# Kernel optimization log

Measured on AMD Instinct MI355X. Metric: run time of the kernel, lower is better.

The kernel has to match this reference:

```python
import jax, jax.numpy as jnp
import numpy as np

C = 64

def _dwconv3d(x, w, b, tdil):
    # x: (B,C,T,H,W); w: (C,1,3,3,3) depthwise; temporal dilation tdil, padding (tdil,1,1)
    y = jax.lax.conv_general_dilated(
        x, w,
        window_strides=(1, 1, 1),
        padding=((tdil, tdil), (1, 1), (1, 1)),
        rhs_dilation=(tdil, 1, 1),
        dimension_numbers=('NCDHW', 'OIDHW', 'NCDHW'),
        feature_group_count=x.shape[1],
    )
    return y + b[None, :, None, None, None]

def _lag_diff(x, k):
    # first k frames kept, rest = x[t] - x[t-k]  (vectorized, no Python loop over T)
    return jnp.concatenate([x[:, :, :k], x[:, :, k:] - x[:, :, :-k]], axis=2)

def setup_inputs() -> dict:
    key = jax.random.key(0)
    ks = jax.random.split(key, 8)
    B, T, H, W = 4, 32, 56, 56
    s = 0.05
    inp = {
        'input': jax.random.normal(ks[0], (B, C, T, H, W), dtype=jnp.float32),
        'w1': jax.random.normal(ks[1], (C, 1, 3, 3, 3), dtype=jnp.float32) * s,
        'b1': jax.random.normal(ks[2], (C,), dtype=jnp.float32) * s,
        'w2': jax.random.normal(ks[3], (C, 1, 3, 3, 3), dtype=jnp.float32) * s,
        'b2': jax.random.normal(ks[4], (C,), dtype=jnp.float32) * s,
        'w3': jax.random.normal(ks[5], (C, 1, 3, 3, 3), dtype=jnp.float32) * s,
        'b3': jax.random.normal(ks[6], (C,), dtype=jnp.float32) * s,
        'weights': jnp.ones((3,), dtype=jnp.float32) / 3.0,
    }
    return inp

def reference(input, w1, b1, w2, b2, w3, b3, weights):
    d1 = _lag_diff(_dwconv3d(input, w1, b1, 1), 1)
    d2 = _lag_diff(_dwconv3d(input, w2, b2, 2), 2)
    d3 = _lag_diff(_dwconv3d(input, w3, b3, 3), 3)
    half = jnp.float32(0.5)
    gate = ((jax.nn.sigmoid(d1) - half) * weights[0]
            + (jax.nn.sigmoid(d2) - half) * weights[1]
            + (jax.nn.sigmoid(d3) - half) * weights[2])
    return input * gate
```

## Files before the change

kernel.cpp:

```cpp
#include <hip/hip_runtime.h>

namespace {

constexpr int T = 32, H = 56, W = 56;
constexpr int HW = H * W;
constexpr int THW = T * HW;
constexpr int PAIRS = HW / 2;
constexpr int BLK = 256;
constexpr int BLOCKS_PER_BC = (PAIRS + BLK - 1) / BLK;

template <int N> struct ic { static constexpr int value = N; };

__device__ __forceinline__ float sigm(float x) {
    float e = __expf(-x);
    return __builtin_amdgcn_rcpf(1.0f + e);
}

__global__ __launch_bounds__(BLK, 4)
void tts_fused(const float* __restrict__ x,
               const float* __restrict__ w1, const float* __restrict__ b1,
               const float* __restrict__ w2, const float* __restrict__ b2,
               const float* __restrict__ w3, const float* __restrict__ b3,
               const float* __restrict__ wm,
               float* __restrict__ out) {
    const int bid = blockIdx.x;
    const int bc  = bid / BLOCKS_PER_BC;
    const int sub = bid - bc * BLOCKS_PER_BC;
    const int q   = sub * BLK + threadIdx.x;
    if (q >= PAIRS) return;
    const int px0 = q * 2;
    const int h   = px0 / W;
    const int w0  = px0 - h * W;

    const float* __restrict__ xbc = x + (size_t)bc * THW;
    float* __restrict__ obc       = out + (size_t)bc * THW;
    const int c = bc & 63;
    const float* __restrict__ wa = w1 + c * 27;
    const float* __restrict__ wb = w2 + c * 27;
    const float* __restrict__ wc = w3 + c * 27;
    const float bias1 = b1[c], bias2 = b2[c], bias3 = b3[c];
    const float W0 = wm[0], W1 = wm[1], W2 = wm[2];
    const float goff = 0.5f * (W0 + W1 + W2);

    const bool vtop = (h >= 1), vbot = (h <= H - 2);
    const bool vl = (w0 > 0), vr = (w0 < W - 2);
    const int boff = h * W + w0;

    float cc[7][3][4];
    float p1[2], p2a[2], p2b[2], p3a[2], p3b[2], p3c[2];
#pragma unroll
    for (int p = 0; p < 2; ++p) {
        p1[p] = 0.f; p2a[p] = 0.f; p2b[p] = 0.f;
        p3a[p] = 0.f; p3b[p] = 0.f; p3c[p] = 0.f;
    }

    auto zero_plane = [&](auto Sc) {
        constexpr int s = decltype(Sc)::value;
#pragma unroll
        for (int r = 0; r < 3; ++r)
#pragma unroll
            for (int j = 0; j < 4; ++j) cc[s][r][j] = 0.f;
    };

    auto load_plane = [&](auto Sc, int tp) {
        constexpr int s = decltype(Sc)::value;
        const float* pp = xbc + tp * HW + boff;
#pragma unroll
        for (int r = 0; r < 3; ++r) {
            const bool vrow = (r == 0) ? vtop : ((r == 2) ? vbot : true);
            const float* rp = pp + (r - 1) * W;
            if (vrow) {
                const float2 m = *(const float2*)rp;
                cc[s][r][1] = m.x; cc[s][r][2] = m.y;
                cc[s][r][0] = vl ? rp[-1] : 0.f;
                cc[s][r][3] = vr ? rp[2]  : 0.f;
            } else {
#pragma unroll
                for (int j = 0; j < 4; ++j) cc[s][r][j] = 0.f;
            }
        }
    };

    auto conv9 = [&](float (&acc)[2], auto Sc, const float* __restrict__ wp) {
        constexpr int s = decltype(Sc)::value;
#pragma unroll
        for (int r = 0; r < 3; ++r)
#pragma unroll
            for (int kw = 0; kw < 3; ++kw) {
                const float wg = wp[r * 3 + kw];
#pragma unroll
                for (int p = 0; p < 2; ++p)
                    acc[p] = fmaf(cc[s][r][p + kw], wg, acc[p]);
            }
    };

    zero_plane(ic<4>{}); zero_plane(ic<5>{}); zero_plane(ic<6>{});
    load_plane(ic<0>{}, 0); load_plane(ic<1>{}, 1); load_plane(ic<2>{}, 2);

    auto step = [&](int t, auto Uc) {
        constexpr int u = decltype(Uc)::value;
        constexpr int snew = (u + 3) % 7;
        if (t + 3 < T) load_plane(ic<snew>{}, t + 3);
        else           zero_plane(ic<snew>{});

        float a1[2], a2[2], a3[2];
#pragma unroll
        for (int p = 0; p < 2; ++p) { a1[p] = bias1; a2[p] = bias2; a3[p] = bias3; }

        conv9(a1, ic<(u + 6) % 7>{}, wa);
        conv9(a1, ic<u>{},           wa + 9);
        conv9(a1, ic<(u + 1) % 7>{}, wa + 18);
        conv9(a2, ic<(u + 5) % 7>{}, wb);
        conv9(a2, ic<u>{},           wb + 9);
        conv9(a2, ic<(u + 2) % 7>{}, wb + 18);
        conv9(a3, ic<(u + 4) % 7>{}, wc);
        conv9(a3, ic<u>{},           wc + 9);
        conv9(a3, ic<(u + 3) % 7>{}, wc + 18);

        float2 ov;
        float* ovp = (float*)&ov;
#pragma unroll
        for (int p = 0; p < 2; ++p) {
            const float y1 = a1[p], y2 = a2[p], y3 = a3[p];
            const float d1 = (t >= 1) ? y1 - p1[p]  : y1;
            const float d2 = (t >= 2) ? y2 - p2b[p] : y2;
            const float d3 = (t >= 3) ? y3 - p3c[p] : y3;
            p1[p]  = y1;
            p2b[p] = p2a[p]; p2a[p] = y2;
            p3c[p] = p3b[p]; p3b[p] = p3a[p]; p3a[p] = y3;
            const float g = fmaf(sigm(d1), W0,
                            fmaf(sigm(d2), W1,
                            fmaf(sigm(d3), W2, -goff)));
            ovp[p] = cc[u][1][p + 1] * g;
        }
        *(float2*)(obc + t * HW + boff) = ov;
    };

#pragma unroll 1
    for (int tb = 0; tb <= T - 7; tb += 7) {
        step(tb + 0, ic<0>{}); step(tb + 1, ic<1>{}); step(tb + 2, ic<2>{});
        step(tb + 3, ic<3>{}); step(tb + 4, ic<4>{}); step(tb + 5, ic<5>{});
        step(tb + 6, ic<6>{});
    }
    step(28, ic<0>{}); step(29, ic<1>{}); step(30, ic<2>{}); step(31, ic<3>{});
}

}

extern "C" void kernel_launch(void* const* d_in, const int* in_sizes, int n_in,
                              void* d_out, int out_size, void* d_ws, size_t ws_size,
                              hipStream_t stream) {
    (void)in_sizes; (void)n_in; (void)d_ws; (void)ws_size; (void)out_size;
    const float* x  = (const float*)d_in[0];
    const float* w1 = (const float*)d_in[1];
    const float* b1 = (const float*)d_in[2];
    const float* w2 = (const float*)d_in[3];
    const float* b2 = (const float*)d_in[4];
    const float* w3 = (const float*)d_in[5];
    const float* b3 = (const float*)d_in[6];
    const float* wm = (const float*)d_in[7];
    float* out = (float*)d_out;

    tts_fused<<<dim3(256 * BLOCKS_PER_BC), dim3(BLK), 0, stream>>>(
        x, w1, b1, w2, b2, w3, b3, wm, out);
}
```

Before: 294.8 us.

## Restructure temporal conv as scatter-accumulate with rolling accumulators and branchless loads

Replaces the 7-plane register ring buffer (gather form) with a scatter form: each input plane is loaded once and its contributions are accumulated into rolling per-output partial sums for all three dilations. Outputs are emitted with a 3-step delay and gate partials are carried forward. Edge loads become branchless clamped offsets with selects, and the block size drops from 256 to 128. The aim is lower register pressure and fewer divergent branches, but the loop is no longer unrolled, so it adds register-shift moves and per-iteration weight loads.

Measured after the change: 298.7 us. About the same (+1.3%).

```diff
diff --git a/kernel.cpp b/kernel.cpp
--- a/kernel.cpp
+++ b/kernel.cpp
@@ -6,14 +6,42 @@
 constexpr int HW = H * W;
 constexpr int THW = T * HW;
 constexpr int PAIRS = HW / 2;
-constexpr int BLK = 256;
-constexpr int BLOCKS_PER_BC = (PAIRS + BLK - 1) / BLK;
+constexpr int BLK = 128;
+constexpr int BPB = (PAIRS + BLK - 1) / BLK;
 
-template <int N> struct ic { static constexpr int value = N; };
+struct F2 { float x, y; };
+struct R4 { float c0, c1, c2, c3; };
 
-__device__ __forceinline__ float sigm(float x) {
-    float e = __expf(-x);
-    return __builtin_amdgcn_rcpf(1.0f + e);
+__device__ __forceinline__ F2 f2(float v) { F2 r; r.x = v; r.y = v; return r; }
+
+__device__ __forceinline__ float sigm(float v) {
+    return __builtin_amdgcn_rcpf(1.0f + __expf(-v));
+}
+
+__device__ __forceinline__ void acc9(F2& a, const R4& r0, const R4& r1, const R4& r2,
+                                     const float* __restrict__ w9) {
+    const float k00 = w9[0], k01 = w9[1], k02 = w9[2];
+    const float k10 = w9[3], k11 = w9[4], k12 = w9[5];
+    const float k20 = w9[6], k21 = w9[7], k22 = w9[8];
+    a.x = fmaf(r0.c0, k00, fmaf(r0.c1, k01, fmaf(r0.c2, k02, a.x)));
+    a.y = fmaf(r0.c1, k00, fmaf(r0.c2, k01, fmaf(r0.c3, k02, a.y)));
+    a.x = fmaf(r1.c0, k10, fmaf(r1.c1, k11, fmaf(r1.c2, k12, a.x)));
+    a.y = fmaf(r1.c1, k10, fmaf(r1.c2, k11, fmaf(r1.c3, k12, a.y)));
+    a.x = fmaf(r2.c0, k20, fmaf(r2.c1, k21, fmaf(r2.c2, k22, a.x)));
+    a.y = fmaf(r2.c1, k20, fmaf(r2.c2, k21, fmaf(r2.c3, k22, a.y)));
+}
+
+__device__ __forceinline__ R4 load_row(const float* __restrict__ p, bool vrow,
+                                       bool vl, bool vr, int cl, int cr) {
+    R4 r;
+    const float2 m = *(const float2*)p;
+    const float e0 = p[cl];
+    const float e3 = p[cr];
+    r.c0 = (vrow && vl) ? e0  : 0.f;
+    r.c1 = vrow         ? m.x : 0.f;
+    r.c2 = vrow         ? m.y : 0.f;
+    r.c3 = (vrow && vr) ? e3  : 0.f;
+    return r;
 }
 
 __global__ __launch_bounds__(BLK, 4)
@@ -24,16 +52,16 @@
                const float* __restrict__ wm,
                float* __restrict__ out) {
     const int bid = blockIdx.x;
-    const int bc  = bid / BLOCKS_PER_BC;
-    const int sub = bid - bc * BLOCKS_PER_BC;
+    const int bc  = bid / BPB;
+    const int sub = bid - bc * BPB;
     const int q   = sub * BLK + threadIdx.x;
     if (q >= PAIRS) return;
     const int px0 = q * 2;
     const int h   = px0 / W;
     const int w0  = px0 - h * W;
 
-    const float* __restrict__ xbc = x + (size_t)bc * THW;
-    float* __restrict__ obc       = out + (size_t)bc * THW;
+    const float* __restrict__ xb = x + (size_t)bc * THW;
+    float* __restrict__ ob       = out + (size_t)bc * THW;
     const int c = bc & 63;
     const float* __restrict__ wa = w1 + c * 27;
     const float* __restrict__ wb = w2 + c * 27;
@@ -42,107 +70,84 @@
     const float W0 = wm[0], W1 = wm[1], W2 = wm[2];
     const float goff = 0.5f * (W0 + W1 + W2);
 
-    const bool vtop = (h >= 1), vbot = (h <= H - 2);
+    const bool vt = (h > 0), vbm = (h < H - 1);
     const bool vl = (w0 > 0), vr = (w0 < W - 2);
-    const int boff = h * W + w0;
+    const int base = h * W + w0;
+    const int ro0 = vt  ? -W : 0;
+    const int ro2 = vbm ?  W : 0;
+    const int cl  = vl ? -1 : 0;
+    const int cr  = vr ? 2 : 0;
 
-    float cc[7][3][4];
-    float p1[2], p2a[2], p2b[2], p3a[2], p3b[2], p3c[2];
-#pragma unroll
-    for (int p = 0; p < 2; ++p) {
-        p1[p] = 0.f; p2a[p] = 0.f; p2b[p] = 0.f;
-        p3a[p] = 0.f; p3b[p] = 0.f; p3c[p] = 0.f;
-    }
+    F2 a1_0 = f2(bias1), a1_1 = f2(bias1), a1_2 = f2(bias1);
+    F2 a2_0 = f2(bias2), a2_1 = f2(bias2), a2_2 = f2(bias2), a2_3 = f2(bias2),
+       a2_4 = f2(bias2);
+    F2 a3_0 = f2(bias3), a3_1 = f2(bias3), a3_2 = f2(bias3), a3_3 = f2(bias3),
+       a3_4 = f2(bias3), a3_5 = f2(bias3), a3_6 = f2(bias3);
+    F2 c1p = f2(0.f), c2p1 = f2(0.f), c2p2 = f2(0.f);
+    F2 c3p1 = f2(0.f), c3p2 = f2(0.f), c3p3 = f2(0.f);
+    F2 gM = f2(0.f), gO = f2(0.f);
+    F2 xc1 = f2(0.f), xc2 = f2(0.f), xc3 = f2(0.f);
 
-    auto zero_plane = [&](auto Sc) {
-        constexpr int s = decltype(Sc)::value;
-#pragma unroll
-        for (int r = 0; r < 3; ++r)
-#pragma unroll
-            for (int j = 0; j < 4; ++j) cc[s][r][j] = 0.f;
-    };
-
-    auto load_plane = [&](auto Sc, int tp) {
-        constexpr int s = decltype(Sc)::value;
-        const float* pp = xbc + tp * HW + boff;
-#pragma unroll
-        for (int r = 0; r < 3; ++r) {
-            const bool vrow = (r == 0) ? vtop : ((r == 2) ? vbot : true);
-            const float* rp = pp + (r - 1) * W;
-            if (vrow) {
-                const float2 m = *(const float2*)rp;
-                cc[s][r][1] = m.x; cc[s][r][2] = m.y;
-                cc[s][r][0] = vl ? rp[-1] : 0.f;
-                cc[s][r][3] = vr ? rp[2]  : 0.f;
-            } else {
-#pragma unroll
-                for (int j = 0; j < 4; ++j) cc[s][r][j] = 0.f;
-            }
-        }
-    };
-
-    auto conv9 = [&](float (&acc)[2], auto Sc, const float* __restrict__ wp) {
-        constexpr int s = decltype(Sc)::value;
-#pragma unroll
-        for (int r = 0; r < 3; ++r)
-#pragma unroll
-            for (int kw = 0; kw < 3; ++kw) {
-                const float wg = wp[r * 3 + kw];
-#pragma unroll
-                for (int p = 0; p < 2; ++p)
-                    acc[p] = fmaf(cc[s][r][p + kw], wg, acc[p]);
-            }
-    };
-
-    zero_plane(ic<4>{}); zero_plane(ic<5>{}); zero_plane(ic<6>{});
-    load_plane(ic<0>{}, 0); load_plane(ic<1>{}, 1); load_plane(ic<2>{}, 2);
-
-    auto step = [&](int t, auto Uc) {
-        constexpr int u = decltype(Uc)::value;
-        constexpr int snew = (u + 3) % 7;
-        if (t + 3 < T) load_plane(ic<snew>{}, t + 3);
-        else           zero_plane(ic<snew>{});
-
-        float a1[2], a2[2], a3[2];
-#pragma unroll
-        for (int p = 0; p < 2; ++p) { a1[p] = bias1; a2[p] = bias2; a3[p] = bias3; }
-
-        conv9(a1, ic<(u + 6) % 7>{}, wa);
-        conv9(a1, ic<u>{},           wa + 9);
-        conv9(a1, ic<(u + 1) % 7>{}, wa + 18);
-        conv9(a2, ic<(u + 5) % 7>{}, wb);
-        conv9(a2, ic<u>{},           wb + 9);
-        conv9(a2, ic<(u + 2) % 7>{}, wb + 18);
-        conv9(a3, ic<(u + 4) % 7>{}, wc);
-        conv9(a3, ic<u>{},           wc + 9);
-        conv9(a3, ic<(u + 3) % 7>{}, wc + 18);
-
-        float2 ov;
-        float* ovp = (float*)&ov;
-#pragma unroll
-        for (int p = 0; p < 2; ++p) {
-            const float y1 = a1[p], y2 = a2[p], y3 = a3[p];
-            const float d1 = (t >= 1) ? y1 - p1[p]  : y1;
-            const float d2 = (t >= 2) ? y2 - p2b[p] : y2;
-            const float d3 = (t >= 3) ? y3 - p3c[p] : y3;
-            p1[p]  = y1;
-            p2b[p] = p2a[p]; p2a[p] = y2;
-            p3c[p] = p3b[p]; p3b[p] = p3a[p]; p3a[p] = y3;
-            const float g = fmaf(sigm(d1), W0,
-                            fmaf(sigm(d2), W1,
-                            fmaf(sigm(d3), W2, -goff)));
-            ovp[p] = cc[u][1][p + 1] * g;
-        }
-        *(float2*)(obc + t * HW + boff) = ov;
-    };
+    int poff = base;
+    int ooff = base;
 
 #pragma unroll 1
-    for (int tb = 0; tb <= T - 7; tb += 7) {
-        step(tb + 0, ic<0>{}); step(tb + 1, ic<1>{}); step(tb + 2, ic<2>{});
-        step(tb + 3, ic<3>{}); step(tb + 4, ic<4>{}); step(tb + 5, ic<5>{});
-        step(tb + 6, ic<6>{});
+    for (int s = 0; s < T + 3; ++s) {
+        R4 r0, r1, r2;
+        if (s < T) {
+            const float* ps = xb + poff;
+            r0 = load_row(ps + ro0, vt,   vl, vr, cl, cr);
+            r1 = load_row(ps,       true, vl, vr, cl, cr);
+            r2 = load_row(ps + ro2, vbm,  vl, vr, cl, cr);
+            poff += HW;
+        } else {
+            r0.c0 = r0.c1 = r0.c2 = r0.c3 = 0.f;
+            r1 = r0; r2 = r0;
+        }
+
+        acc9(a1_2, r0, r1, r2, wa);
+        acc9(a1_1, r0, r1, r2, wa + 9);
+        acc9(a1_0, r0, r1, r2, wa + 18);
+        acc9(a2_4, r0, r1, r2, wb);
+        acc9(a2_2, r0, r1, r2, wb + 9);
+        acc9(a2_0, r0, r1, r2, wb + 18);
+        acc9(a3_6, r0, r1, r2, wc);
+        acc9(a3_3, r0, r1, r2, wc + 9);
+        acc9(a3_0, r0, r1, r2, wc + 18);
+
+        const F2 c1 = a1_0, c2 = a2_0, c3 = a3_0;
+        F2 d1, d2, d3;
+        if (s >= 2) { d1.x = c1.x - c1p.x;  d1.y = c1.y - c1p.y;  } else d1 = c1;
+        if (s >= 4) { d2.x = c2.x - c2p2.x; d2.y = c2.y - c2p2.y; } else d2 = c2;
+        if (s >= 6) { d3.x = c3.x - c3p3.x; d3.y = c3.y - c3p3.y; } else d3 = c3;
+
+        F2 s1v, s2v, s3v;
+        s1v.x = sigm(d1.x) * W0; s1v.y = sigm(d1.y) * W0;
+        s2v.x = sigm(d2.x) * W1; s2v.y = sigm(d2.y) * W1;
+        s3v.x = sigm(d3.x) * W2; s3v.y = sigm(d3.y) * W2;
+
+        if (s >= 3) {
+            float2 ov;
+            ov.x = xc3.x * (gO.x + s3v.x - goff);
+            ov.y = xc3.y * (gO.y + s3v.y - goff);
+            *(float2*)(ob + ooff) = ov;
+            ooff += HW;
+        }
+        gO.x = gM.x + s2v.x; gO.y = gM.y + s2v.y;
+        gM = s1v;
+
+        a1_0 = a1_1; a1_1 = a1_2; a1_2 = f2(bias1);
+        a2_0 = a2_1; a2_1 = a2_2; a2_2 = a2_3; a2_3 = a2_4; a2_4 = f2(bias2);
+        a3_0 = a3_1; a3_1 = a3_2; a3_2 = a3_3; a3_3 = a3_4; a3_4 = a3_5;
+        a3_5 = a3_6; a3_6 = f2(bias3);
+
+        c1p = c1;
+        c2p2 = c2p1; c2p1 = c2;
+        c3p3 = c3p2; c3p2 = c3p1; c3p1 = c3;
+
+        xc3 = xc2; xc2 = xc1;
+        xc1.x = r1.c1; xc1.y = r1.c2;
     }
-    step(28, ic<0>{}); step(29, ic<1>{}); step(30, ic<2>{}); step(31, ic<3>{});
 }
 
 }
@@ -161,6 +166,6 @@
     const float* wm = (const float*)d_in[7];
     float* out = (float*)d_out;
 
-    tts_fused<<<dim3(256 * BLOCKS_PER_BC), dim3(BLK), 0, stream>>>(
+    tts_fused<<<dim3(256 * BPB), dim3(BLK), 0, stream>>>(
         x, w1, b1, w2, b2, w3, b3, wm, out);
 }
```
